# Kernel optimization log

Measured on AMD Instinct MI355X. Metric: run time of the kernel, lower is better.

The kernel has to match this reference:

```python
import jax, jax.numpy as jnp
import numpy as np

H, D = 4, 32
HID = H * D  # 128
NA, NW, NO = 100_000, 20_000, 50_000
E = 150_000
OFFS = (0, NA, NA + NW, NA + NW + NO)
NTOT = OFFS[3]
# node order: assignments=0, workers=1, orders=2
# edge types (src_type, dst_type): w->a, o->a, a->w, a->o
ETYPES = ((1, 0), (2, 0), (0, 1), (0, 2))


def setup_inputs() -> dict:
    key = jax.random.key(0)
    ks = jax.random.split(key, 20)
    s = 0.05
    return {
        "x_a": jax.random.normal(ks[0], (NA, 64), jnp.float32),
        "x_w": jax.random.normal(ks[1], (NW, 64), jnp.float32),
        "x_o": jax.random.normal(ks[2], (NO, 64), jnp.float32),
        "W_in": jax.random.normal(ks[3], (3, 64, HID), jnp.float32) * s,
        "b_in": jnp.zeros((3, HID), jnp.float32),
        "W_kqv": jax.random.normal(ks[4], (2, 3, HID, 3 * HID), jnp.float32) * s,
        "b_kqv": jnp.zeros((2, 3, 3 * HID), jnp.float32),
        "a_rel": jax.random.normal(ks[5], (2, 4, H, D, D), jnp.float32) * s,
        "m_rel": jax.random.normal(ks[6], (2, 4, H, D, D), jnp.float32) * s,
        "p_rel": jnp.ones((2, 4, H), jnp.float32),
        "skip_p": jnp.ones((2, 3), jnp.float32),
        "W_o": jax.random.normal(ks[7], (2, 3, HID, HID), jnp.float32) * s,
        "b_o": jnp.zeros((2, 3, HID), jnp.float32),
        "ln_g": jnp.ones((2, 3, HID), jnp.float32),
        "ln_b": jnp.zeros((2, 3, HID), jnp.float32),
        "w_head": jax.random.normal(ks[8], (HID, 1), jnp.float32) * s,
        "b_head": jnp.zeros((1,), jnp.float32),
        "base": jnp.zeros((1,), jnp.float32),
        "src_wa": jax.random.randint(ks[9], (E,), 0, NW),
        "dst_wa": jax.random.randint(ks[10], (E,), 0, NA),
        "src_oa": jax.random.randint(ks[11], (E,), 0, NO),
        "dst_oa": jax.random.randint(ks[12], (E,), 0, NA),
        "src_aw": jax.random.randint(ks[13], (E,), 0, NA),
        "dst_aw": jax.random.randint(ks[14], (E,), 0, NW),
        "src_ao": jax.random.randint(ks[15], (E,), 0, NA),
        "dst_ao": jax.random.randint(ks[16], (E,), 0, NO),
    }


def _ln(x, g, b):
    mu = jnp.mean(x, axis=-1, keepdims=True)
    var = jnp.var(x, axis=-1, keepdims=True)
    return (x - mu) * jax.lax.rsqrt(var + 1e-5) * g + b


def _hgt_forward(x_a, x_w, x_o, W_in, b_in, W_kqv, b_kqv, a_rel, m_rel, p_rel,
                 skip_p, W_o, b_o, ln_g, ln_b, w_head, b_head, base, edges):
    # input projection + relu per node type
    xs = [jax.nn.relu(x @ W_in[t] + b_in[t]) for t, x in enumerate((x_a, x_w, x_o))]
    scale = 1.0 / np.sqrt(D).astype(np.float32)
    for l in range(2):  # num_layers (structurally distinct params)
        # per-node-type fused K/Q/V projection (PyG kqv_lin)
        kqv = [xs[t] @ W_kqv[l, t] + b_kqv[l, t] for t in range(3)]
        kd = [m[:, :HID].reshape(-1, H, D) for m in kqv]
        qd = [m[:, HID:2 * HID].reshape(-1, H, D) for m in kqv]
        vd = [m[:, 2 * HID:].reshape(-1, H, D) for m in kqv]
        alphas, vals, dsts = [], [], []
        for e, (st, dt) in enumerate(ETYPES):  # 4 relation types
            src, dst = edges[e]
            # per-edge-type per-head relation transforms applied at node level
            ke = jnp.einsum('nhd,hde->nhe', kd[st], a_rel[l, e])
            ve = jnp.einsum('nhd,hde->nhe', vd[st], m_rel[l, e])
            kg = ke[src]            # [E,H,D] gather
            vg = ve[src]
            qg = qd[dt][dst]
            alphas.append((qg * kg).sum(-1) * p_rel[l, e] * scale)  # [E,H]
            vals.append(vg)
            dsts.append(OFFS[dt] + dst)
        alpha = jnp.concatenate(alphas, axis=0)   # [Etot,H]
        vall = jnp.concatenate(vals, axis=0)      # [Etot,H,D]
        dstg = jnp.concatenate(dsts, axis=0)      # [Etot]
        # segment softmax over all incoming edges of each destination node
        amax = jax.ops.segment_max(alpha, dstg, num_segments=NTOT)
        ex = jnp.exp(alpha - amax[dstg])
        den = jax.ops.segment_sum(ex, dstg, num_segments=NTOT)
        w = ex / (den[dstg] + 1e-16)
        agg = jax.ops.segment_sum(w[:, :, None] * vall, dstg, num_segments=NTOT)
        agg = agg.reshape(NTOT, HID)
        new_xs = []
        for t in range(3):
            o = agg[OFFS[t]:OFFS[t + 1]]
            o = jax.nn.gelu(o, approximate=False) @ W_o[l, t] + b_o[l, t]
            g = jax.nn.sigmoid(skip_p[l, t])
            o = g * o + (1.0 - g) * xs[t]
            new_xs.append(jax.nn.relu(_ln(o, ln_g[l, t], ln_b[l, t])))
        xs = new_xs
    delta = (xs[0] @ w_head)[:, 0] + b_head[0]
    return base[0] + delta  # [NA]


def reference(x_a, x_w, x_o, W_in, b_in, W_kqv, b_kqv, a_rel, m_rel, p_rel,
              skip_p, W_o, b_o, ln_g, ln_b, w_head, b_head, base,
              src_wa, dst_wa, src_oa, dst_oa, src_aw, dst_aw, src_ao, dst_ao):
    edges = ((src_wa, dst_wa), (src_oa, dst_oa), (src_aw, dst_aw), (src_ao, dst_ao))
    return _hgt_forward(x_a, x_w, x_o, W_in, b_in, W_kqv, b_kqv, a_rel, m_rel,
                        p_rel, skip_p, W_o, b_o, ln_g, ln_b, w_head, b_head,
                        base, edges)
```

## Files before the change

kernel.cpp:

```cpp
#include <hip/hip_runtime.h>
#include <cstddef>
#include <cmath>

namespace {

constexpr int H = 4, D = 32, HID = 128;
constexpr int NA = 100000, NW = 20000, NO = 50000;
constexpr int NTOT = NA + NW + NO;
constexpr int E = 150000;
constexpr float SCALE = 0.17677669529663687f;
constexpr int LDK = 3 * HID;

typedef __attribute__((ext_vector_type(8))) short short8v;
typedef __attribute__((ext_vector_type(4))) float f32x4;

__device__ __forceinline__ float gelu_exact(float x) {
  return 0.5f * x * (1.f + erff(x * 0.7071067811865475f));
}
__device__ __forceinline__ unsigned short f2bf(float f) {
  unsigned u = __float_as_uint(f);
  return (unsigned short)((u + 0x7FFF + ((u >> 16) & 1)) >> 16);
}
__device__ __forceinline__ float bf2f(unsigned short s) {
  return __uint_as_float(((unsigned)s) << 16);
}
__device__ __forceinline__ float blo(unsigned w) {
  return __uint_as_float(w << 16);
}
__device__ __forceinline__ float bhi(unsigned w) {
  return __uint_as_float(w & 0xFFFF0000u);
}

__device__ __forceinline__ int btype(int bx, int nb0, int nb01) {
  return bx < nb0 ? 0 : (bx < nb01 ? 1 : 2);
}

template <int KSTEPS, bool A_FP32>
__device__ __forceinline__ void gemm_body(
    const void* __restrict__ Av, int lda, const unsigned short* __restrict__ BT,
    int ldb, f32x4* acc, int M, int bm) {
  __shared__ unsigned short As[64 * 64];
  __shared__ unsigned short Bs[128 * 64];
  const int tid = threadIdx.x;
  const int wv = tid >> 6, l = tid & 63;
  for (int ks = 0; ks < KSTEPS; ks++) {
    const int kk = ks * 64;
    #pragma unroll
    for (int p = 0; p < 2; p++) {
      int idx = tid + p * 256;
      int r = idx >> 3, c = idx & 7;
      int gr = bm + r;
      unsigned short tmp[8] = {0, 0, 0, 0, 0, 0, 0, 0};
      if (gr < M) {
        if (A_FP32) {
          const float* src = (const float*)Av + (size_t)gr * lda + kk + c * 8;
          float4 f0 = *(const float4*)src;
          float4 f1 = *(const float4*)(src + 4);
          tmp[0] = f2bf(f0.x); tmp[1] = f2bf(f0.y);
          tmp[2] = f2bf(f0.z); tmp[3] = f2bf(f0.w);
          tmp[4] = f2bf(f1.x); tmp[5] = f2bf(f1.y);
          tmp[6] = f2bf(f1.z); tmp[7] = f2bf(f1.w);
        } else {
          *(uint4*)tmp = *(const uint4*)((const unsigned short*)Av +
                                         (size_t)gr * lda + kk + c * 8);
        }
      }
      *(uint4*)&As[r * 64 + ((c ^ (r & 7)) * 8)] = *(const uint4*)tmp;
    }
    #pragma unroll
    for (int p = 0; p < 4; p++) {
      int idx = tid + p * 256;
      int r = idx >> 3, c = idx & 7;
      uint4 v = *(const uint4*)(BT + (size_t)r * ldb + kk + c * 8);
      *(uint4*)&Bs[r * 64 + ((c ^ (r & 7)) * 8)] = v;
    }
    __syncthreads();
    const int arow = wv * 16 + (l & 15);
    #pragma unroll
    for (int ksub = 0; ksub < 2; ksub++) {
      int ch = ksub * 4 + (l >> 4);
      short8v af = *(const short8v*)&As[arow * 64 + ((ch ^ (arow & 7)) * 8)];
      #pragma unroll
      for (int n = 0; n < 8; n++) {
        int brow = n * 16 + (l & 15);
        short8v bf =
            *(const short8v*)&Bs[brow * 64 + ((ch ^ (brow & 7)) * 8)];
        acc[n] =
            __builtin_amdgcn_mfma_f32_16x16x32_bf16(af, bf, acc[n], 0, 0, 0);
      }
    }
    __syncthreads();
  }
}

__global__ __launch_bounds__(256) void prep_weights(
    const float* __restrict__ W_in, const float* __restrict__ W_kqv,
    const float* __restrict__ W_o, unsigned short* __restrict__ WinT,
    unsigned short* __restrict__ Wk0T, unsigned short* __restrict__ WoT) {
  int idx = blockIdx.x * 256 + threadIdx.x;
  const int N1 = 3 * 128 * 64, N2 = 2 * 384 * 128, N3 = 6 * 128 * 128;
  if (idx < N1) {
    int t = idx / 8192, rem = idx - t * 8192;
    int n = rem >> 6, k = rem & 63;
    WinT[idx] = f2bf(W_in[(size_t)t * 64 * 128 + (size_t)k * 128 + n]);
  } else if (idx < N1 + N2) {
    int r = idx - N1;
    int lyr = r / (384 * 128), rem = r - lyr * (384 * 128);
    int n = rem >> 7, k = rem & 127;
    Wk0T[r] = f2bf(W_kqv[(size_t)lyr * 3 * 128 * 384 + (size_t)k * 384 + n]);
  } else if (idx < N1 + N2 + N3) {
    int r = idx - N1 - N2;
    int lt = r / (128 * 128), rem = r - lt * (128 * 128);
    int n = rem >> 7, k = rem & 127;
    WoT[r] = f2bf(W_o[(size_t)lt * 128 * 128 + (size_t)k * 128 + n]);
  }
}

__global__ __launch_bounds__(256) void fold_weights2(
    const float* __restrict__ W_kqv, const float* __restrict__ b_kqv,
    const float* __restrict__ a_rel, const float* __restrict__ m_rel,
    unsigned short* __restrict__ WeT, float* __restrict__ be) {
  const int lyr = blockIdx.y;
  const size_t DD = (size_t)H * D * D;
  const float* Wl = W_kqv + (size_t)lyr * 3 * HID * LDK;
  const float* bl = b_kqv + (size_t)lyr * 3 * LDK;
  const float* Al = a_rel + (size_t)lyr * 4 * DD;
  const float* Ml = m_rel + (size_t)lyr * 4 * DD;
  unsigned short* WeTl = WeT + (size_t)lyr * 2 * 384 * 128;
  float* bel = be + (size_t)lyr * 2 * 384;
  int idx = blockIdx.x * 256 + threadIdx.x;
  const int NW_ = 2 * 128 * 384;
  if (idx < NW_) {
    int tt = idx / (128 * 384);
    int rem = idx - tt * (128 * 384);
    int r = rem / 384, c = rem - r * 384;
    int slice = c >> 7, h = (c >> 5) & 3, j = c & 31;
    const float* Wsrc = Wl + (size_t)(tt + 1) * 128 * 384 + (size_t)r * 384;
    float acc = 0.f;
    if (slice == 0) {
      const float* A = Al + ((size_t)tt * H + h) * D * D;
      for (int d = 0; d < 32; d++) acc += Wsrc[h * 32 + d] * A[d * 32 + j];
    } else if (slice == 1) {
      const float* A = Al + ((size_t)(2 + tt) * H + h) * D * D;
      for (int e = 0; e < 32; e++)
        acc += Wsrc[128 + h * 32 + e] * A[j * 32 + e];
    } else {
      const float* Mm = Ml + ((size_t)tt * H + h) * D * D;
      for (int d = 0; d < 32; d++)
        acc += Wsrc[256 + h * 32 + d] * Mm[d * 32 + j];
    }
    WeTl[(size_t)tt * 384 * 128 + (size_t)c * 128 + r] = f2bf(acc);
  } else if (idx < NW_ + 2 * 384) {
    int rem = idx - NW_;
    int tt = rem / 384, c = rem - tt * 384;
    int slice = c >> 7, h = (c >> 5) & 3, j = c & 31;
    const float* bsrc = bl + (size_t)(tt + 1) * 384;
    float acc = 0.f;
    if (slice == 0) {
      const float* A = Al + ((size_t)tt * H + h) * D * D;
      for (int d = 0; d < 32; d++) acc += bsrc[h * 32 + d] * A[d * 32 + j];
    } else if (slice == 1) {
      const float* A = Al + ((size_t)(2 + tt) * H + h) * D * D;
      for (int e = 0; e < 32; e++)
        acc += bsrc[128 + h * 32 + e] * A[j * 32 + e];
    } else {
      const float* Mm = Ml + ((size_t)tt * H + h) * D * D;
      for (int d = 0; d < 32; d++)
        acc += bsrc[256 + h * 32 + d] * Mm[d * 32 + j];
    }
    bel[rem] = acc;
  }
}

__global__ __launch_bounds__(256) void in_fused(
    const float* __restrict__ xa, const float* __restrict__ xw,
    const float* __restrict__ xo, const unsigned short* __restrict__ WinT,
    const float* __restrict__ b_in, unsigned short* __restrict__ xs, int nb0,
    int nb01) {
  int t = btype(blockIdx.x, nb0, nb01);
  int base = t == 0 ? 0 : (t == 1 ? nb0 : nb01);
  int M = t == 0 ? NA : (t == 1 ? NW : NO);
  int off = t == 0 ? 0 : (t == 1 ? NA : NA + NW);
  const float* A = t == 0 ? xa : (t == 1 ? xw : xo);
  const int bm = (blockIdx.x - base) * 64;
  f32x4 acc[8] = {};
  gemm_body<1, true>(A, 64, WinT + (size_t)t * 128 * 64, 64, acc, M, bm);
  const int l = threadIdx.x & 63, wv = threadIdx.x >> 6;
  const float* bias = b_in + t * HID;
  unsigned short* C = xs + (size_t)off * HID;
  #pragma unroll
  for (int n = 0; n < 8; n++) {
    int col = n * 16 + (l & 15);
    float bb = bias[col];
    #pragma unroll
    for (int j = 0; j < 4; j++) {
      int row = bm + wv * 16 + (l >> 4) * 4 + j;
      if (row < M) C[(size_t)row * HID + col] = f2bf(fmaxf(acc[n][j] + bb, 0.f));
    }
  }
}

__global__ __launch_bounds__(256) void kqv_fused(
    const unsigned short* __restrict__ xs, const unsigned short* __restrict__ Wk0Tl,
    const float* __restrict__ b0, const unsigned short* __restrict__ WeT,
    const float* __restrict__ be, unsigned short* __restrict__ kqvB, int nb0,
    int nb01) {
  __shared__ unsigned short As[64 * 128];
  __shared__ unsigned short Bs[128 * 128];
  int t = btype(blockIdx.x, nb0, nb01);
  int base = t == 0 ? 0 : (t == 1 ? nb0 : nb01);
  int M = t == 0 ? NA : (t == 1 ? NW : NO);
  int off = t == 0 ? 0 : (t == 1 ? NA : NA + NW);
  const unsigned short* BT =
      (t == 0 ? Wk0Tl : WeT + (size_t)(t - 1) * 384 * 128);
  const float* bias = t == 0 ? b0 : be + (size_t)(t - 1) * 384;
  const int bm = (blockIdx.x - base) * 64;
  const int tid = threadIdx.x;
  const int wv = tid >> 6, l = tid & 63;
  #pragma unroll
  for (int p = 0; p < 4; p++) {
    int idx = tid + p * 256;
    int r = idx >> 4, c = idx & 15;
    int gr = bm + r;
    uint4 v = {0, 0, 0, 0};
    if (gr < M)
      v = *(const uint4*)(xs + (size_t)(off + gr) * HID + c * 8);
    *(uint4*)&As[r * 128 + ((c ^ (r & 15)) * 8)] = v;
  }
  const int arow = wv * 16 + (l & 15);
  unsigned short* C = kqvB + (size_t)off * LDK;
  for (int bn = 0; bn < 384; bn += 128) {
    if (bn) __syncthreads();
    #pragma unroll
    for (int p = 0; p < 8; p++) {
      int idx = tid + p * 256;
      int r = idx >> 4, c = idx & 15;
      uint4 v = *(const uint4*)(BT + (size_t)(bn + r) * 128 + c * 8);
      *(uint4*)&Bs[r * 128 + ((c ^ (r & 15)) * 8)] = v;
    }
    __syncthreads();
    f32x4 acc[8] = {};
    #pragma unroll
    for (int ks = 0; ks < 4; ks++) {
      int ch = ks * 4 + (l >> 4);
      short8v af = *(const short8v*)&As[arow * 128 + ((ch ^ (arow & 15)) * 8)];
      #pragma unroll
      for (int n = 0; n < 8; n++) {
        int brow = n * 16 + (l & 15);
        short8v bf =
            *(const short8v*)&Bs[brow * 128 + ((ch ^ (brow & 15)) * 8)];
        acc[n] =
            __builtin_amdgcn_mfma_f32_16x16x32_bf16(af, bf, acc[n], 0, 0, 0);
      }
    }
    #pragma unroll
    for (int n = 0; n < 8; n++) {
      int col = bn + n * 16 + (l & 15);
      float bb = bias[col];
      #pragma unroll
      for (int j = 0; j < 4; j++) {
        int row = bm + wv * 16 + (l >> 4) * 4 + j;
        if (row < M) C[(size_t)row * LDK + col] = f2bf(acc[n][j] + bb);
      }
    }
  }
}

__global__ __launch_bounds__(256) void wo_ln_fused(
    const unsigned short* __restrict__ kqvB, const unsigned short* __restrict__ WoTl,
    const float* __restrict__ bl, unsigned short* __restrict__ xs,
    const float* __restrict__ skipl, const float* __restrict__ gll,
    const float* __restrict__ bll, int nb0, int nb01, int doHead,
    const float* __restrict__ w_head, const float* __restrict__ b_head,
    const float* __restrict__ basep, float* __restrict__ outHead) {
  int t = btype(blockIdx.x, nb0, nb01);
  int base = t == 0 ? 0 : (t == 1 ? nb0 : nb01);
  int M = t == 0 ? NA : (t == 1 ? NW : NO);
  int off = t == 0 ? 0 : (t == 1 ? NA : NA + NW);
  const int bm = (blockIdx.x - base) * 64;
  f32x4 acc[8] = {};
  gemm_body<2, false>(kqvB + (size_t)off * LDK + HID, LDK,
                      WoTl + (size_t)t * 128 * 128, 128, acc, M, bm);
  const int l = threadIdx.x & 63, wv = threadIdx.x >> 6;
  const float* bias = bl + t * HID;
  const float* gln = gll + t * HID;
  const float* bln = bll + t * HID;
  unsigned short* xsT = xs + (size_t)off * HID;
  const float g = 1.f / (1.f + expf(-skipl[t]));
  const bool hd = (doHead != 0) && (t == 0);
  float bb[8], gl8[8], bl8[8], wh8[8];
  #pragma unroll
  for (int n = 0; n < 8; n++) {
    int col = n * 16 + (l & 15);
    bb[n] = bias[col];
    gl8[n] = gln[col];
    bl8[n] = bln[col];
    wh8[n] = hd ? w_head[col] : 0.f;
  }
  #pragma unroll
  for (int j = 0; j < 4; j++) {
    int row = bm + wv * 16 + (l >> 4) * 4 + j;
    bool ok = row < M;
    float vv[8], sum = 0.f, sq = 0.f;
    #pragma unroll
    for (int n = 0; n < 8; n++) {
      int col = n * 16 + (l & 15);
      float xo = ok ? bf2f(xsT[(size_t)row * HID + col]) : 0.f;
      float val = g * (acc[n][j] + bb[n]) + (1.f - g) * xo;
      vv[n] = val;
      sum += val;
      sq += val * val;
    }
    #pragma unroll
    for (int m = 1; m < 16; m <<= 1) {
      sum += __shfl_xor(sum, m, 64);
      sq += __shfl_xor(sq, m, 64);
    }
    float mu = sum * (1.f / 128.f);
    float var = sq * (1.f / 128.f) - mu * mu;
    float r = rsqrtf(var + 1e-5f);
    if (ok) {
      float dot = 0.f;
      #pragma unroll
      for (int n = 0; n < 8; n++) {
        float y = fmaxf((vv[n] - mu) * r * gl8[n] + bl8[n], 0.f);
        xsT[(size_t)row * HID + n * 16 + (l & 15)] = f2bf(y);
        dot += bf2f(f2bf(y)) * wh8[n];
      }
      if (hd) {
        dot += __shfl_xor(dot, 1, 64);
        dot += __shfl_xor(dot, 2, 64);
        dot += __shfl_xor(dot, 4, 64);
        dot += __shfl_xor(dot, 8, 64);
        if ((l & 15) == 0) outHead[row] = basep[0] + b_head[0] + dot;
      }
    }
  }
}

__global__ __launch_bounds__(256) void csr_hist4(
    const int* __restrict__ d0, const int* __restrict__ d1,
    const int* __restrict__ d2, const int* __restrict__ d3,
    int* __restrict__ cnt) {
  int t = blockIdx.x * 256 + threadIdx.x;
  if (t >= 4 * E) return;
  int et = t / E, e = t - et * E;
  const int* dp = et == 0 ? d0 : et == 1 ? d1 : et == 2 ? d2 : d3;
  int base = et == 0 ? 0 : et == 1 ? NA : et == 2 ? 2 * NA : 2 * NA + NW;
  atomicAdd(&cnt[base + dp[e]], 1);
}

__global__ __launch_bounds__(256) void scan_block_all(
    const int* __restrict__ cnt, int* __restrict__ rpAll,
    int* __restrict__ bsum) {
  const int nbA = (NA + 255) / 256, nbW = (NW + 255) / 256,
            nbO = (NO + 255) / 256;
  int bx = blockIdx.x;
  int et, bbase, cbase, rpo, n;
  if (bx < nbA) { et = 0; bbase = 0; cbase = 0; rpo = 0; n = NA; }
  else if (bx < 2 * nbA) { et = 1; bbase = nbA; cbase = NA; rpo = NA + 1; n = NA; }
  else if (bx < 2 * nbA + nbW) {
    et = 2; bbase = 2 * nbA; cbase = 2 * NA; rpo = 2 * (NA + 1); n = NW;
  } else {
    et = 3; bbase = 2 * nbA + nbW; cbase = 2 * NA + NW;
    rpo = 2 * (NA + 1) + (NW + 1); n = NO;
  }
  int lb = bx - bbase;
  __shared__ int tmp[256];
  int i = lb * 256 + threadIdx.x;
  int v = (i < n) ? cnt[cbase + i] : 0;
  tmp[threadIdx.x] = v;
  __syncthreads();
  int acc = v;
  for (int off = 1; off < 256; off <<= 1) {
    int other = (threadIdx.x >= off) ? tmp[threadIdx.x - off] : 0;
    __syncthreads();
    acc += other;
    tmp[threadIdx.x] = acc;
    __syncthreads();
  }
  if (i < n) rpAll[rpo + i] = acc - v;
  if (threadIdx.x == 255) bsum[et * 512 + lb] = acc;
}

__global__ __launch_bounds__(256) void scan_bsums_all(int* __restrict__ bsum) {
  int et = blockIdx.x;
  int nb = et < 2 ? (NA + 255) / 256 : (et == 2 ? (NW + 255) / 256
                                                : (NO + 255) / 256);
  int* bs = bsum + et * 512;
  __shared__ int tmp[256];
  __shared__ int carry;
  if (threadIdx.x == 0) carry = 0;
  __syncthreads();
  for (int start = 0; start < nb; start += 256) {
    int i = start + threadIdx.x;
    int v = (i < nb) ? bs[i] : 0;
    tmp[threadIdx.x] = v;
    __syncthreads();
    int acc = v;
    for (int off = 1; off < 256; off <<= 1) {
      int other = (threadIdx.x >= off) ? tmp[threadIdx.x - off] : 0;
      __syncthreads();
      acc += other;
      tmp[threadIdx.x] = acc;
      __syncthreads();
    }
    int c = carry;
    if (i < nb) bs[i] = c + acc - v;
    __syncthreads();
    if (threadIdx.x == 255) carry = c + acc;
    __syncthreads();
  }
}

__device__ __forceinline__ void et_of_node(int i, int& et, int& base, int& nd,
                                           int& rpo) {
  if (i < NA) { et = 0; base = 0; nd = NA; rpo = 0; }
  else if (i < 2 * NA) { et = 1; base = NA; nd = NA; rpo = NA + 1; }
  else if (i < 2 * NA + NW) { et = 2; base = 2 * NA; nd = NW; rpo = 2 * (NA + 1); }
  else { et = 3; base = 2 * NA + NW; nd = NO; rpo = 2 * (NA + 1) + NW + 1; }
}

__global__ __launch_bounds__(256) void csr_finalize4(
    int* __restrict__ rpAll, const int* __restrict__ bsum,
    int* __restrict__ cursor) {
  int i = blockIdx.x * 256 + threadIdx.x;
  if (i >= 2 * NA + NW + NO) return;
  int et, base, nd, rpo;
  et_of_node(i, et, base, nd, rpo);
  int local = i - base;
  int v = rpAll[rpo + local] + bsum[et * 512 + (local >> 8)];
  rpAll[rpo + local] = v;
  cursor[base + local] = v;
  if (local == 0) rpAll[rpo + nd] = E;
}

__global__ __launch_bounds__(256) void csr_scatter4(
    const int* __restrict__ d0, const int* __restrict__ d1,
    const int* __restrict__ d2, const int* __restrict__ d3,
    int* __restrict__ cursor, int* __restrict__ ceAll) {
  int t = blockIdx.x * 256 + threadIdx.x;
  if (t >= 4 * E) return;
  int et = t / E, e = t - et * E;
  const int* dp = et == 0 ? d0 : et == 1 ? d1 : et == 2 ? d2 : d3;
  int base = et == 0 ? 0 : et == 1 ? NA : et == 2 ? 2 * NA : 2 * NA + NW;
  int slot = atomicAdd(&cursor[base + dp[e]], 1);
  ceAll[(size_t)et * E + slot] = e;
}

__global__ __launch_bounds__(256) void csr_finish(
    const int* __restrict__ rpAll, int* __restrict__ ceAll,
    const int* __restrict__ s0, const int* __restrict__ s1,
    const int* __restrict__ s2, const int* __restrict__ s3,
    int* __restrict__ srcOf, int* __restrict__ descI) {
  int i = blockIdx.x * 256 + threadIdx.x;
  if (i >= 2 * NA + NW + NO) return;
  int et, base, nd, rpo;
  et_of_node(i, et, base, nd, rpo);
  int local = i - base;
  int b = rpAll[rpo + local], e = rpAll[rpo + local + 1];
  int* ce = ceAll + (size_t)et * E;
  for (int k = b + 1; k < e; k++) {
    int key = ce[k];
    int j = k - 1;
    while (j >= b && ce[j] > key) { ce[j + 1] = ce[j]; j--; }
    ce[j + 1] = key;
  }
  const int* sp = et == 0 ? s0 : et == 1 ? s1 : et == 2 ? s2 : s3;
  int sOff = et == 0 ? NA : et == 1 ? NA + NW : 0;
  int* so = srcOf + (size_t)et * E;
  for (int k = b; k < e; k++) so[k] = sOff + sp[ce[k]];
  if (et == 0) {
    descI[(size_t)local * 4 + 0] = b;
    descI[(size_t)local * 4 + 1] = e;
  } else if (et == 1) {
    descI[(size_t)local * 4 + 2] = b;
    descI[(size_t)local * 4 + 3] = e;
  } else {
    int dl = (et == 2) ? NA + local : NA + NW + local;
    descI[(size_t)dl * 4 + 0] = b;
    descI[(size_t)dl * 4 + 1] = e;
    descI[(size_t)dl * 4 + 2] = 0;
    descI[(size_t)dl * 4 + 3] = 0;
  }
}

__global__ __launch_bounds__(256) void attn_fused(
    const unsigned short* __restrict__ kqv, const int4* __restrict__ desc,
    const int* __restrict__ srcOf, const float* __restrict__ Pl,
    const float* __restrict__ Ml, unsigned short* __restrict__ out) {
  int dl = (blockIdx.x * 256 + threadIdx.x) >> 6;
  int lane = threadIdx.x & 63;
  if (dl >= NTOT) return;
  int q = lane >> 4, p = lane & 15;
  int4 dd = desc[dl];
  int b0 = dd.x, e0 = dd.y, b1 = dd.z, e1 = dd.w;
  int et23 = -1;
  const int* so0;
  const int* so1 = srcOf;
  float ps0, ps1 = 0.f;
  if (dl < NA) {
    so0 = srcOf; so1 = srcOf + E;
    ps0 = Pl[q] * SCALE; ps1 = Pl[H + q] * SCALE;
  } else if (dl < NA + NW) {
    so0 = srcOf + 2 * (size_t)E;
    ps0 = Pl[2 * H + q] * SCALE;
    et23 = 2;
  } else {
    so0 = srcOf + 3 * (size_t)E;
    ps0 = Pl[3 * H + q] * SCALE;
    et23 = 3;
  }
  const int n0 = e0 - b0;
  const int n01 = n0 + (e1 - b1);
  auto srcAt = [&](int t) -> int {
    return (t < n0) ? so0[b0 + t] : so1[b1 + (t - n0)];
  };
  unsigned qv = *(const unsigned*)(kqv + (size_t)dl * LDK + HID + lane * 2);
  float qx = blo(qv), qy = bhi(qv);
  const int lo2 = lane * 2;

  float m = -INFINITY, den = 0.f, ax = 0.f, ay = 0.f;
  unsigned ka = 0, va = 0, kb = 0, vb = 0;
  int i2 = 0, i3 = 0;
  if (n01 > 0) {
    const unsigned short* r = kqv + (size_t)srcAt(0) * LDK;
    ka = *(const unsigned*)(r + lo2);
    va = *(const unsigned*)(r + 2 * HID + lo2);
  }
  if (n01 > 1) {
    const unsigned short* r = kqv + (size_t)srcAt(1) * LDK;
    kb = *(const unsigned*)(r + lo2);
    vb = *(const unsigned*)(r + 2 * HID + lo2);
  }
  if (n01 > 2) i2 = srcAt(2);
  if (n01 > 3) i3 = srcAt(3);
  int t = 0;
  for (; t + 1 < n01; t += 2) {
    unsigned pka = ka, pva = va, pkb = kb, pvb = vb;
    float psa = (t < n0) ? ps0 : ps1;
    float psb = (t + 1 < n0) ? ps0 : ps1;
    if (t + 2 < n01) {
      const unsigned short* r = kqv + (size_t)i2 * LDK;
      ka = *(const unsigned*)(r + lo2);
      va = *(const unsigned*)(r + 2 * HID + lo2);
    }
    if (t + 3 < n01) {
      const unsigned short* r = kqv + (size_t)i3 * LDK;
      kb = *(const unsigned*)(r + lo2);
      vb = *(const unsigned*)(r + 2 * HID + lo2);
    }
    if (t + 4 < n01) i2 = srcAt(t + 4);
    if (t + 5 < n01) i3 = srcAt(t + 5);
    float sa = qx * blo(pka) + qy * bhi(pka);
    float sb = qx * blo(pkb) + qy * bhi(pkb);
    sa += __shfl_xor(sa, 1, 64);
    sb += __shfl_xor(sb, 1, 64);
    sa += __shfl_xor(sa, 2, 64);
    sb += __shfl_xor(sb, 2, 64);
    sa += __shfl_xor(sa, 4, 64);
    sb += __shfl_xor(sb, 4, 64);
    sa += __shfl_xor(sa, 8, 64);
    sb += __shfl_xor(sb, 8, 64);
    sa *= psa;
    sb *= psb;
    float nm = fmaxf(m, fmaxf(sa, sb));
    float c = __expf(m - nm);
    float wa = __expf(sa - nm), wb = __expf(sb - nm);
    den = den * c + wa + wb;
    ax = ax * c + wa * blo(pva) + wb * blo(pvb);
    ay = ay * c + wa * bhi(pva) + wb * bhi(pvb);
    m = nm;
  }
  if (t < n01) {
    float ps = (t < n0) ? ps0 : ps1;
    float s = qx * blo(ka) + qy * bhi(ka);
    s += __shfl_xor(s, 1, 64);
    s += __shfl_xor(s, 2, 64);
    s += __shfl_xor(s, 4, 64);
    s += __shfl_xor(s, 8, 64);
    s *= ps;
    float nm = fmaxf(m, s);
    float c = __expf(m - nm);
    float w = __expf(s - nm);
    den = den * c + w;
    ax = ax * c + w * blo(va);
    ay = ay * c + w * bhi(va);
  }
  float inv = 1.f / (den + 1e-16f);
  ax *= inv;
  ay *= inv;
  if (et23 >= 0) {
    const float* Mm = Ml + ((size_t)et23 * H + q) * D * D;
    int base = lane & 48;
    float o0 = 0.f, o1 = 0.f;
    #pragma unroll
    for (int j = 0; j < 16; j++) {
      float s0 = __shfl(ax, base + j, 64);
      float s1 = __shfl(ay, base + j, 64);
      float2 m0 = *(const float2*)&Mm[(2 * j) * 32 + 2 * p];
      float2 m1 = *(const float2*)&Mm[(2 * j + 1) * 32 + 2 * p];
      o0 += s0 * m0.x + s1 * m1.x;
      o1 += s0 * m0.y + s1 * m1.y;
    }
    ax = o0; ay = o1;
  }
  unsigned ov = (unsigned)f2bf(gelu_exact(ax)) |
                ((unsigned)f2bf(gelu_exact(ay)) << 16);
  *(unsigned*)(out + (size_t)dl * LDK + HID + lane * 2) = ov;
}

}

extern "C" void kernel_launch(void* const* d_in, const int* in_sizes, int n_in,
                              void* d_out, int out_size, void* d_ws,
                              size_t ws_size, hipStream_t stream) {
  const float* x_a = (const float*)d_in[0];
  const float* x_w = (const float*)d_in[1];
  const float* x_o = (const float*)d_in[2];
  const float* W_in = (const float*)d_in[3];
  const float* b_in = (const float*)d_in[4];
  const float* W_kqv = (const float*)d_in[5];
  const float* b_kqv = (const float*)d_in[6];
  const float* a_rel = (const float*)d_in[7];
  const float* m_rel = (const float*)d_in[8];
  const float* p_rel = (const float*)d_in[9];
  const float* skip_p = (const float*)d_in[10];
  const float* W_o = (const float*)d_in[11];
  const float* b_o = (const float*)d_in[12];
  const float* ln_g = (const float*)d_in[13];
  const float* ln_b = (const float*)d_in[14];
  const float* w_head = (const float*)d_in[15];
  const float* b_head = (const float*)d_in[16];
  const float* basep = (const float*)d_in[17];
  const int* srcs[4] = {(const int*)d_in[18], (const int*)d_in[20],
                        (const int*)d_in[22], (const int*)d_in[24]};
  const int* dsts[4] = {(const int*)d_in[19], (const int*)d_in[21],
                        (const int*)d_in[23], (const int*)d_in[25]};

  const size_t SZ_XS = (size_t)NTOT * HID * 2;
  const size_t SZ_KQV = (size_t)NTOT * LDK * 2;
  const size_t SZ_WINT = (size_t)3 * 128 * 64 * 2;
  const size_t SZ_WK0T = (size_t)2 * 384 * 128 * 2;
  const size_t SZ_WOT = (size_t)6 * 128 * 128 * 2;
  const size_t SZ_WET = (size_t)2 * 2 * 384 * 128 * 2;
  const size_t SZ_BE = ((size_t)2 * 2 * 384 * 4 + 63) & ~63ull;
  const size_t SZ_SD = (size_t)4 * E * 4;
  const size_t SZ_DESC = (size_t)NTOT * 16;
  const int CNT_TOT = 2 * NA + NW + NO;
  const int RP_TOT = 2 * (NA + 1) + (NW + 1) + (NO + 1);
  const size_t SZ_RP = ((size_t)RP_TOT * 4 + 63) & ~63ull;
  const size_t SZ_CE = (size_t)4 * E * 4;
  const size_t SZ_CU = ((size_t)CNT_TOT * 4 + 63) & ~63ull;
  const size_t SZ_BS = 4 * 512 * 4;
  const size_t need = SZ_XS + SZ_KQV + SZ_WINT + SZ_WK0T + SZ_WOT + SZ_WET +
                      SZ_BE + SZ_SD + SZ_DESC + SZ_RP + SZ_CE + 2 * SZ_CU +
                      SZ_BS;
  if (ws_size < need) return;

  char* p = (char*)d_ws;
  unsigned short* xs = (unsigned short*)p;    p += SZ_XS;
  unsigned short* kqvB = (unsigned short*)p;  p += SZ_KQV;
  unsigned short* WinT = (unsigned short*)p;  p += SZ_WINT;
  unsigned short* Wk0T = (unsigned short*)p;  p += SZ_WK0T;
  unsigned short* WoT = (unsigned short*)p;   p += SZ_WOT;
  unsigned short* WeT = (unsigned short*)p;   p += SZ_WET;
  float* beB = (float*)p;                     p += SZ_BE;
  int* srcOf = (int*)p;                       p += SZ_SD;
  int4* descB = (int4*)p;                     p += SZ_DESC;
  int* rpAll = (int*)p;                       p += SZ_RP;
  int* ceAll = (int*)p;                       p += SZ_CE;
  int* cursor = (int*)p;                      p += SZ_CU;
  int* cnt = (int*)p;                         p += SZ_CU;
  int* bsum = (int*)p;

  const int CNTT = 2 * NA + NW + NO;
  const int e4b = (4 * E + 255) / 256;
  const int nb0 = (NA + 63) / 64, nb01 = nb0 + (NW + 63) / 64;
  const int nbTot = nb01 + (NO + 63) / 64;
  const int nbA = (NA + 255) / 256, nbW = (NW + 255) / 256,
            nbO = (NO + 255) / 256;

  hipMemsetAsync(cnt, 0, (size_t)CNTT * 4, stream);
  csr_hist4<<<e4b, 256, 0, stream>>>(dsts[0], dsts[1], dsts[2], dsts[3], cnt);
  scan_block_all<<<2 * nbA + nbW + nbO, 256, 0, stream>>>(cnt, rpAll, bsum);
  scan_bsums_all<<<4, 256, 0, stream>>>(bsum);
  csr_finalize4<<<(CNTT + 255) / 256, 256, 0, stream>>>(rpAll, bsum, cursor);
  csr_scatter4<<<e4b, 256, 0, stream>>>(dsts[0], dsts[1], dsts[2], dsts[3],
                                        cursor, ceAll);
  csr_finish<<<(CNTT + 255) / 256, 256, 0, stream>>>(
      rpAll, ceAll, srcs[0], srcs[1], srcs[2], srcs[3], srcOf, (int*)descB);

  prep_weights<<<(3 * 128 * 64 + 2 * 384 * 128 + 6 * 128 * 128 + 255) / 256,
                 256, 0, stream>>>(W_in, W_kqv, W_o, WinT, Wk0T, WoT);
  fold_weights2<<<dim3((2 * 128 * 384 + 2 * 384 + 255) / 256, 2), 256, 0,
                  stream>>>(W_kqv, b_kqv, a_rel, m_rel, WeT, beB);
  in_fused<<<nbTot, 256, 0, stream>>>(x_a, x_w, x_o, WinT, b_in, xs, nb0, nb01);

  const size_t DD = (size_t)H * D * D;
  for (int l = 0; l < 2; l++) {
    const float* Ml = m_rel + (size_t)l * 4 * DD;
    const float* Pl = p_rel + (size_t)l * 4 * H;
    const float* bl = b_kqv + (size_t)l * 3 * LDK;
    kqv_fused<<<nbTot, 256, 0, stream>>>(
        xs, Wk0T + (size_t)l * 384 * 128, bl,
        WeT + (size_t)l * 2 * 384 * 128, beB + (size_t)l * 2 * 384, kqvB, nb0,
        nb01);
    attn_fused<<<(NTOT + 3) / 4, 256, 0, stream>>>(kqvB, descB, srcOf, Pl, Ml,
                                                   kqvB);
    wo_ln_fused<<<nbTot, 256, 0, stream>>>(
        kqvB, WoT + (size_t)l * 3 * 128 * 128, b_o + (size_t)l * 3 * HID, xs,
        skip_p + l * 3, ln_g + (size_t)l * 3 * HID, ln_b + (size_t)l * 3 * HID,
        nb0, nb01, (l == 1) ? 1 : 0, w_head, b_head, basep, (float*)d_out);
  }
}
```

Measured before the change: 661.0 us.

## Sort destination nodes by in-degree to balance attention wavefront work

Adds a counting-sort pass (histogram, scan, scatter) that builds a permutation of destination nodes grouped by total in-degree. The attention kernel then maps each wavefront to a permuted node, so wavefronts in a block handle nodes of similar degree and spend less time idling at divergent loop ends. The cost is three extra small kernels plus a memset, and an indirect load per wavefront. Atomic scatter order within a bin also breaks the spatial locality of the output and kqv writes.

```diff
diff --git a/kernel.cpp b/kernel.cpp
--- a/kernel.cpp
+++ b/kernel.cpp
@@ -10,6 +10,7 @@
 constexpr int E = 150000;
 constexpr float SCALE = 0.17677669529663687f;
 constexpr int LDK = 3 * HID;
+constexpr int NBINS = 64;
 
 typedef __attribute__((ext_vector_type(8))) short short8v;
 typedef __attribute__((ext_vector_type(4))) float f32x4;
@@ -485,13 +486,55 @@
   }
 }
 
+__global__ __launch_bounds__(256) void deg_hist(const int4* __restrict__ desc,
+                                                int* __restrict__ bins) {
+  int dl = blockIdx.x * 256 + threadIdx.x;
+  if (dl >= NTOT) return;
+  int4 d = desc[dl];
+  int deg = (d.y - d.x) + (d.w - d.z);
+  int b = deg < NBINS ? deg : NBINS - 1;
+  atomicAdd(&bins[b], 1);
+}
+
+__global__ __launch_bounds__(64) void bin_scan(const int* __restrict__ bins,
+                                               int* __restrict__ binCur) {
+  __shared__ int tmp[NBINS];
+  int i = threadIdx.x;
+  int v = bins[i];
+  tmp[i] = v;
+  __syncthreads();
+  int acc = v;
+  for (int off = 1; off < NBINS; off <<= 1) {
+    int other = (i >= off) ? tmp[i - off] : 0;
+    __syncthreads();
+    acc += other;
+    tmp[i] = acc;
+    __syncthreads();
+  }
+  binCur[i] = acc - v;
+}
+
+__global__ __launch_bounds__(256) void deg_scatter(
+    const int4* __restrict__ desc, int* __restrict__ binCur,
+    int* __restrict__ perm) {
+  int dl = blockIdx.x * 256 + threadIdx.x;
+  if (dl >= NTOT) return;
+  int4 d = desc[dl];
+  int deg = (d.y - d.x) + (d.w - d.z);
+  int b = deg < NBINS ? deg : NBINS - 1;
+  int pos = atomicAdd(&binCur[b], 1);
+  perm[pos] = dl;
+}
+
 __global__ __launch_bounds__(256) void attn_fused(
     const unsigned short* __restrict__ kqv, const int4* __restrict__ desc,
     const int* __restrict__ srcOf, const float* __restrict__ Pl,
-    const float* __restrict__ Ml, unsigned short* __restrict__ out) {
-  int dl = (blockIdx.x * 256 + threadIdx.x) >> 6;
+    const float* __restrict__ Ml, const int* __restrict__ perm,
+    unsigned short* __restrict__ out) {
+  int gw = (blockIdx.x * 256 + threadIdx.x) >> 6;
   int lane = threadIdx.x & 63;
-  if (dl >= NTOT) return;
+  if (gw >= NTOT) return;
+  int dl = perm[gw];
   int q = lane >> 4, p = lane & 15;
   int4 dd = desc[dl];
   int b0 = dd.x, e0 = dd.y, b1 = dd.z, e1 = dd.w;
@@ -647,6 +690,8 @@
   const size_t SZ_BE = ((size_t)2 * 2 * 384 * 4 + 63) & ~63ull;
   const size_t SZ_SD = (size_t)4 * E * 4;
   const size_t SZ_DESC = (size_t)NTOT * 16;
+  const size_t SZ_PERM = ((size_t)NTOT * 4 + 63) & ~63ull;
+  const size_t SZ_BIN = ((size_t)2 * NBINS * 4 + 63) & ~63ull;
   const int CNT_TOT = 2 * NA + NW + NO;
   const int RP_TOT = 2 * (NA + 1) + (NW + 1) + (NO + 1);
   const size_t SZ_RP = ((size_t)RP_TOT * 4 + 63) & ~63ull;
@@ -654,8 +699,8 @@
   const size_t SZ_CU = ((size_t)CNT_TOT * 4 + 63) & ~63ull;
   const size_t SZ_BS = 4 * 512 * 4;
   const size_t need = SZ_XS + SZ_KQV + SZ_WINT + SZ_WK0T + SZ_WOT + SZ_WET +
-                      SZ_BE + SZ_SD + SZ_DESC + SZ_RP + SZ_CE + 2 * SZ_CU +
-                      SZ_BS;
+                      SZ_BE + SZ_SD + SZ_DESC + SZ_PERM + SZ_BIN + SZ_RP +
+                      SZ_CE + 2 * SZ_CU + SZ_BS;
   if (ws_size < need) return;
 
   char* p = (char*)d_ws;
@@ -668,6 +713,8 @@
   float* beB = (float*)p;                     p += SZ_BE;
   int* srcOf = (int*)p;                       p += SZ_SD;
   int4* descB = (int4*)p;                     p += SZ_DESC;
+  int* permB = (int*)p;                       p += SZ_PERM;
+  int* binsB = (int*)p;                       p += SZ_BIN;
   int* rpAll = (int*)p;                       p += SZ_RP;
   int* ceAll = (int*)p;                       p += SZ_CE;
   int* cursor = (int*)p;                      p += SZ_CU;
@@ -690,6 +737,11 @@
                                         cursor, ceAll);
   csr_finish<<<(CNTT + 255) / 256, 256, 0, stream>>>(
       rpAll, ceAll, srcs[0], srcs[1], srcs[2], srcs[3], srcOf, (int*)descB);
+  hipMemsetAsync(binsB, 0, (size_t)NBINS * 4, stream);
+  deg_hist<<<(NTOT + 255) / 256, 256, 0, stream>>>(descB, binsB);
+  bin_scan<<<1, NBINS, 0, stream>>>(binsB, binsB + NBINS);
+  deg_scatter<<<(NTOT + 255) / 256, 256, 0, stream>>>(descB, binsB + NBINS,
+                                                      permB);
 
   prep_weights<<<(3 * 128 * 64 + 2 * 384 * 128 + 6 * 128 * 128 + 255) / 256,
                  256, 0, stream>>>(W_in, W_kqv, W_o, WinT, Wk0T, WoT);
@@ -707,7 +759,7 @@
         WeT + (size_t)l * 2 * 384 * 128, beB + (size_t)l * 2 * 384, kqvB, nb0,
         nb01);
     attn_fused<<<(NTOT + 3) / 4, 256, 0, stream>>>(kqvB, descB, srcOf, Pl, Ml,
-                                                   kqvB);
+                                                   permB, kqvB);
     wo_ln_fused<<<nbTot, 256, 0, stream>>>(
         kqvB, WoT + (size_t)l * 3 * 128 * 128, b_o + (size_t)l * 3 * HID, xs,
         skip_p + l * 3, ln_g + (size_t)l * 3 * HID, ln_b + (size_t)l * 3 * HID,
```

New measurement: 2.145 ms. 224% more time.
